# Kernel optimization log

Measured on AMD Instinct MI355X. Metric: run time of the kernel, lower is better.

Reference implementation:

```python
import jax, jax.numpy as jnp
import numpy as np

N_NODES = 50000
EPS_NORM = 1e-12
EPS_ENT = 1e-8

def _l2norm(x):
    # torch.nn.functional.normalize: x / clamp(||x||, min=1e-12)
    n = jnp.sqrt(jnp.sum(x * x, axis=-1, keepdims=True))
    return x / jnp.maximum(n, EPS_NORM)

def _layer(hidden, src, dst, edge_type, multi_emb, proto_emb):
    # hidden: [N,H]; multi_emb: [R,P,H]; proto_emb: [P,H]
    inp_j = hidden[src]                          # [E,H] gather
    rel_basis = multi_emb[edge_type]             # [E,P,H] gather
    sims = jnp.einsum('eh,ph->ep', _l2norm(inp_j), _l2norm(proto_emb))  # cosine sim [E,P]
    proto_proba = jax.nn.softmax(sims, axis=1)   # [E,P]
    msg = jnp.einsum('ep,eph->eh', proto_proba, rel_basis)              # [E,H]
    ent = -jnp.sum(proto_proba * jnp.log(proto_proba + EPS_ENT), axis=1)  # [E]
    logits = -ent
    # scatter_softmax over destination index
    seg_max = jax.ops.segment_max(logits, dst, num_segments=N_NODES)
    ex = jnp.exp(logits - seg_max[dst])
    denom = jax.ops.segment_sum(ex, dst, num_segments=N_NODES)
    attn = ex / denom[dst]                       # [E]
    out = jax.ops.segment_sum(attn[:, None] * msg, dst, num_segments=N_NODES)  # [N,H]
    return out

def setup_inputs() -> dict:
    key = jax.random.key(0)
    ks = jax.random.split(key, 6)
    E = 800000
    H, R, P, L = 128, 18, 18, 3  # num_layers=4 -> 3 NBFCluttr layers
    edge_index = jax.random.randint(ks[0], (2, E), 0, N_NODES, dtype=jnp.int64) if jax.config.read('jax_enable_x64') else jax.random.randint(ks[0], (2, E), 0, N_NODES, dtype=jnp.int32)
    edge_type = jax.random.randint(ks[1], (E,), 0, R, dtype=edge_index.dtype)
    tail_indices = jax.random.randint(ks[2], (1024,), 0, N_NODES, dtype=edge_index.dtype)
    multi_embeddings = jax.random.uniform(ks[3], (L, R, P, H), dtype=jnp.float32)
    proto_embeddings = jax.random.uniform(ks[4], (L, P, H), dtype=jnp.float32)
    source_embedding = jax.random.uniform(ks[5], (H,), dtype=jnp.float32)
    return {"edge_index": edge_index, "edge_type": edge_type, "tail_indices": tail_indices,
            "multi_embeddings": multi_embeddings, "proto_embeddings": proto_embeddings,
            "source_embedding": source_embedding}

def reference(edge_index, edge_type, tail_indices, multi_embeddings, proto_embeddings, source_embedding):
    src, dst = edge_index[0], edge_index[1]
    H = source_embedding.shape[0]
    # boundary condition: source node gets source_embedding, rest zero
    hidden = jnp.zeros((N_NODES, H), dtype=source_embedding.dtype).at[0].set(source_embedding)
    L = multi_embeddings.shape[0]
    for l in range(L):  # small fixed loop over structurally distinct layers
        hidden = _layer(hidden, src, dst, edge_type, multi_embeddings[l], proto_embeddings[l])
    # apply_classifier, eval_mode=True, use_mlp_classifier=False -> cosine sims to last layer prototypes
    out_emb = hidden[tail_indices]               # [B,H]
    sims = jnp.einsum('nh,ph->np', _l2norm(out_emb), _l2norm(proto_embeddings[-1]))
    return sims  # gumbel_softmax_sample with eval_mode=True returns logits unchanged
```

## Files before the change

kernel.cpp:

```cpp
#include <hip/hip_runtime.h>
#include <hip/hip_bf16.h>


#define N_NODES 50000
#define H 128
#define P 18
#define RP 324
#define KPAD 352
#define K0PAD 32
#define ELLW 64
#define NPART 8
#define NODES_PER_PART 6250
#define PREP_MAIN_BLOCKS 384
#define PREP_PN_BLOCKS 14
#define PREP_GS_BLOCKS 162
#define N0CAP 1024
#define NEED_CAP 20480

typedef _Float16 half8 __attribute__((ext_vector_type(8)));
typedef _Float16 half2v __attribute__((ext_vector_type(2)));
typedef float floatx4 __attribute__((ext_vector_type(4)));

__global__ __launch_bounds__(256) void ell_kernel(const int* __restrict__ src,
                                                  const int* __restrict__ dst,
                                                  const int* __restrict__ etype,
                                                  unsigned* __restrict__ cur,
                                                  unsigned* __restrict__ ep,
                                                  unsigned* __restrict__ n0list, int E) {
  int part = blockIdx.x & (NPART - 1);
  int i = (blockIdx.x >> 3) * 256 + threadIdx.x;
  if (i >= E) return;
  int d = dst[i];
  int lo = part * NODES_PER_PART;
  if (d < lo || d >= lo + NODES_PER_PART) return;
  int s = src[i];
  int r = etype[i];
  unsigned pos = atomicAdd(&cur[d], 1u);
  if (pos < ELLW)
    ep[(size_t)d * ELLW + pos] = (unsigned)s | ((unsigned)r << 20);
  if (s == 0) {
    unsigned ix = atomicAdd(&cur[N_NODES], 1u);
    if (ix < N0CAP) n0list[ix] = (unsigned)d | ((unsigned)r << 20);
  }
}

__global__ __launch_bounds__(256) void need_kernel(const int* __restrict__ tl,
                                                   const unsigned* __restrict__ ep,
                                                   unsigned* __restrict__ cur,
                                                   unsigned* __restrict__ nflag,
                                                   unsigned* __restrict__ needlist, int T) {
  int wave = threadIdx.x >> 6, lane = threadIdx.x & 63;
  int t = blockIdx.x * 4 + wave;
  if (t >= T) return;
  int nd = tl[t];
  int cnt = (int)cur[nd];
  if (cnt > ELLW) cnt = ELLW;
  if (lane < cnt) {
    unsigned s = ep[(size_t)nd * ELLW + lane] & 0xFFFFFu;
    if (atomicExch(&nflag[s], 1u) == 0u) {
      unsigned ix = atomicAdd(&cur[N_NODES + 1], 1u);
      if (ix < NEED_CAP) needlist[ix] = s;
    }
  }
}

__global__ __launch_bounds__(256) void prep_kernel(const float* __restrict__ multi,
                                                   const float* __restrict__ proto,
                                                   const float* __restrict__ semb,
                                                   float* __restrict__ pN,
                                                   _Float16* __restrict__ Btg,
                                                   _Float16* __restrict__ Btl0,
                                                   _Float16* __restrict__ BtD,
                                                   float* __restrict__ GS,
                                                   unsigned* __restrict__ cur,
                                                   unsigned* __restrict__ nflag) {
  int bid = blockIdx.x;
  if (bid >= PREP_MAIN_BLOCKS + PREP_PN_BLOCKS) {
    int wave = threadIdx.x >> 6, lane = threadIdx.x & 63;
    int pi = (bid - PREP_MAIN_BLOCKS - PREP_PN_BLOCKS) * 4 + wave;
    if (pi >= 648) return;
    float pr = 1.f / 18.f, ent0 = 0.f;
#pragma unroll
    for (int p = 0; p < P; p++) ent0 -= pr * __logf(pr + 1e-8f);
    float qc = __expf(-ent0) * pr;
    bool isG = pi < 324;
    int rr = isG ? pi / P : (pi - 324) / P;
    int cc = isG ? pi - rr * P : (pi - 324) - rr * P;
    float ca = 0.f, cb = 0.f;
#pragma unroll
    for (int q2 = 0; q2 < P; q2++) {
      ca += multi[(rr * P + q2) * H + lane];
      cb += multi[(rr * P + q2) * H + lane + 64];
    }
    ca *= qc; cb *= qc;
    float xa, xb, rn = 0.f;
    if (isG) {
      xa = proto[(P + cc) * H + lane];
      xb = proto[(P + cc) * H + lane + 64];
      rn = xa * xa + xb * xb;
    } else {
      xa = 0.f; xb = 0.f;
#pragma unroll
      for (int q2 = 0; q2 < P; q2++) {
        xa += multi[(cc * P + q2) * H + lane];
        xb += multi[(cc * P + q2) * H + lane + 64];
      }
      xa *= qc; xb *= qc;
    }
    float dotp = ca * xa + cb * xb;
    for (int m = 32; m > 0; m >>= 1) {
      dotp += __shfl_xor(dotp, m, 64);
      rn += __shfl_xor(rn, m, 64);
    }
    float val = isG ? dotp / fmaxf(sqrtf(rn), 1e-12f) : dotp;
    if (lane == 0) GS[pi] = val;
    return;
  }
  if (bid >= PREP_MAIN_BLOCKS) {
    int wave = threadIdx.x >> 6, l = threadIdx.x & 63;
    int row = (bid - PREP_MAIN_BLOCKS) * 4 + wave;
    if (row >= 54) return;
    float a = proto[row * H + l], b = proto[row * H + 64 + l];
    float ss = a * a + b * b;
    for (int m = 32; m > 0; m >>= 1) ss += __shfl_xor(ss, m, 64);
    float inv = 1.f / fmaxf(sqrtf(ss), 1e-12f);
    pN[row * H + l] = a * inv;
    pN[row * H + 64 + l] = b * inv;
    return;
  }
  int idx = bid * 256 + threadIdx.x;
  if (idx <= N_NODES + 1) cur[idx] = 0u;
  if (idx < N_NODES) nflag[idx] = 0u;
  if (idx < 2 * H * KPAD) {
    int l = idx / (H * KPAD), rem = idx - l * (H * KPAD);
    int h = rem / KPAD, k = rem - h * KPAD;
    const float* B = multi + (size_t)(l + 1) * RP * H;
    Btg[idx] = (k < RP) ? (_Float16)B[k * H + h] : (_Float16)0.f;
    return;
  }
  int idx2 = idx - 2 * H * KPAD;
  if (idx2 >= H * 64) return;
  int h = idx2 >> 6, k = idx2 & 63;
  float s0 = semb[k], s1 = semb[k + 64];
  float ssq = s0 * s0 + s1 * s1;
  float dq[P];
#pragma unroll
  for (int p = 0; p < P; p++) {
    float a = proto[p * H + k], b = proto[p * H + 64 + k];
    float rn = a * a + b * b;
    for (int m = 32; m > 0; m >>= 1) rn += __shfl_xor(rn, m, 64);
    float rinv = 1.f / fmaxf(sqrtf(rn), 1e-12f);
    dq[p] = (s0 * a + s1 * b) * rinv;
  }
  for (int m = 1; m <= 32; m <<= 1) {
    ssq += __shfl_xor(ssq, m, 64);
#pragma unroll
    for (int p = 0; p < P; p++) dq[p] += __shfl_xor(dq[p], m, 64);
  }
  float inv = 1.f / fmaxf(sqrtf(ssq), 1e-12f);
  float sum = 0.f;
#pragma unroll
  for (int p = 0; p < P; p++) {
    dq[p] = __expf(dq[p] * inv - 1.f);
    sum += dq[p];
  }
  float isum = 1.f / sum, ent = 0.f;
#pragma unroll
  for (int p = 0; p < P; p++) {
    dq[p] *= isum;
    ent -= dq[p] * __logf(dq[p] + 1e-8f);
  }
  float w = __expf(-ent);
  float pr = 1.f / 18.f, ent0 = 0.f;
#pragma unroll
  for (int p = 0; p < P; p++) ent0 -= pr * __logf(pr + 1e-8f);
  float qc = __expf(-ent0) * pr;
  if (k < K0PAD) {
    float v = 0.f;
    if (k < P) {
#pragma unroll
      for (int p = 0; p < P; p++) v += qc * multi[(k * P + p) * H + h];
    }
    Btl0[h * K0PAD + k] = (_Float16)v;
  } else if (k < K0PAD + P) {
    int r = k - K0PAD;
    float v = 0.f;
#pragma unroll
    for (int p = 0; p < P; p++) v += (w * dq[p] - qc) * multi[(r * P + p) * H + h];
    BtD[r * H + h] = (_Float16)v;
  }
}

__global__ __launch_bounds__(256) void histq_kernel(const unsigned* __restrict__ ep,
                                                    const unsigned* __restrict__ cur,
                                                    const float* __restrict__ GS,
                                                    _Float16* __restrict__ q, int n) {
  __shared__ float gs[648];
  for (int i = threadIdx.x; i < 648; i += 256) gs[i] = GS[i];
  __syncthreads();
  int wave = threadIdx.x >> 6, lane = threadIdx.x & 63;
  int nd = blockIdx.x * 4 + wave;
  if (nd >= n) return;
  int cnt = (int)cur[nd];
  if (cnt > ELLW) cnt = ELLW;
  bool a = lane < cnt;
  unsigned pk = a ? ep[(size_t)nd * ELLW + lane] : 0xFFFFFFFFu;
  int r = (int)(pk >> 20);
  float creg = 0.f;
#pragma unroll
  for (int rr = 0; rr < P; rr++) {
    unsigned long long m = __ballot(a && (r == rr));
    if (lane == rr) creg = (float)__popcll(m);
  }
  float dot = 0.f, t = 0.f;
#pragma unroll
  for (int rr = 0; rr < P; rr++) {
    float c = __shfl(creg, rr, 64);
    if (lane < P) {
      dot += c * gs[rr * P + lane];
      t += c * gs[324 + rr * P + lane];
    }
  }
  float u = (lane < P) ? creg * t : 0.f;
  for (int m = 1; m <= 16; m <<= 1) u += __shfl_xor(u, m, 32);
  float ss = u;
  float inv = 1.f / fmaxf(sqrtf(ss), 1e-12f);
  float e = (lane < P) ? __expf(dot * inv - 1.f) : 0.f;
  float sum = e;
  for (int m = 1; m <= 16; m <<= 1) sum += __shfl_xor(sum, m, 32);
  float prb = e / sum;
  float term = (lane < P) ? prb * __logf(prb + 1e-8f) : 0.f;
  float ent = term;
  for (int m = 1; m <= 16; m <<= 1) ent += __shfl_xor(ent, m, 32);
  float w = __expf(ent);
  if (lane < P) q[(size_t)nd * P + lane] = (_Float16)(w * prb);
}

__global__ __launch_bounds__(256) void patch_kernel(const unsigned* __restrict__ cur,
                                                    const unsigned* __restrict__ n0list,
                                                    const unsigned* __restrict__ ep,
                                                    const _Float16* __restrict__ Btl0,
                                                    const _Float16* __restrict__ BtD,
                                                    const float* __restrict__ pN,
                                                    _Float16* __restrict__ q) {
  int n0 = (int)cur[N_NODES];
  if (n0 > N0CAP) n0 = N0CAP;
  int wave = threadIdx.x >> 6, lane = threadIdx.x & 63;
  int e = blockIdx.x * 4 + wave;
  if (e >= n0) return;
  unsigned pe = n0list[e];
  int d = (int)(pe & 0xFFFFFu);
  for (int e2 = 0; e2 < e; e2++)
    if ((int)(n0list[e2] & 0xFFFFFu) == d) return;
  int cnt = (int)cur[d];
  if (cnt > ELLW) cnt = ELLW;
  bool a = lane < cnt;
  unsigned pk2 = a ? ep[(size_t)d * ELLW + lane] : 0xFFFFFFFFu;
  int rr0 = (int)(pk2 >> 20);
  float creg = 0.f;
#pragma unroll
  for (int rr = 0; rr < P; rr++) {
    unsigned long long m = __ballot(a && (rr0 == rr));
    if (lane == rr) creg = (float)__popcll(m);
  }
  float ya = 0.f, yb = 0.f;
#pragma unroll
  for (int rr = 0; rr < P; rr++) {
    float c = __shfl(creg, rr, 64);
    ya += c * (float)Btl0[lane * K0PAD + rr];
    yb += c * (float)Btl0[(lane + 64) * K0PAD + rr];
  }
  for (int e2 = e; e2 < n0; e2++) {
    unsigned p2 = n0list[e2];
    if ((int)(p2 & 0xFFFFFu) != d) continue;
    int r2 = (int)(p2 >> 20);
    ya += (float)BtD[r2 * H + lane];
    yb += (float)BtD[r2 * H + lane + 64];
  }
  float ss = ya * ya + yb * yb;
  float dot[P];
#pragma unroll
  for (int p = 0; p < P; p++) dot[p] = ya * pN[p * H + lane] + yb * pN[p * H + lane + 64];
  for (int m = 1; m <= 32; m <<= 1) {
    ss += __shfl_xor(ss, m, 64);
#pragma unroll
    for (int p = 0; p < P; p++) dot[p] += __shfl_xor(dot[p], m, 64);
  }
  float inv = 1.f / fmaxf(sqrtf(ss), 1e-12f);
  float sum = 0.f;
#pragma unroll
  for (int p = 0; p < P; p++) {
    dot[p] = __expf(dot[p] * inv - 1.f);
    sum += dot[p];
  }
  float isum = 1.f / sum, ent = 0.f;
#pragma unroll
  for (int p = 0; p < P; p++) {
    dot[p] *= isum;
    ent -= dot[p] * __logf(dot[p] + 1e-8f);
  }
  float w = __expf(-ent);
  if (lane < P) q[(size_t)d * P + lane] = (_Float16)(w * dot[lane]);
}

__global__ __launch_bounds__(256) void scatter_kernel(const unsigned* __restrict__ ep,
                                                      const unsigned* __restrict__ cur,
                                                      const _Float16* __restrict__ q,
                                                      const int* __restrict__ tl,
                                                      const unsigned* __restrict__ dc,
                                                      _Float16* __restrict__ M, int n) {
  __shared__ float sl[4][3 * RP];
  int wave = threadIdx.x >> 6, lane = threadIdx.x & 63;
  int t = blockIdx.x * 4 + wave;
  int neff = n;
  if (dc) {
    int c = (int)dc[0];
    if (c < neff) neff = c;
  }
  float* s0 = sl[wave];
  for (int i = lane; i < 3 * RP; i += 64) s0[i] = 0.f;
  int sub = lane / 18;
  int j = lane - sub * 18;
  bool act = (sub < 3) && (t < neff);
  int cnt = 0;
  size_t b = 0;
  if (t < neff) {
    int nd = tl ? tl[t] : t;
    b = (size_t)nd * ELLW;
    cnt = (int)cur[nd];
    if (cnt > ELLW) cnt = ELLW;
  }
  float* ms = s0 + (sub < 3 ? sub : 0) * RP;
  for (int it = 0; it < cnt; it += 18) {
    bool aa[6];
    unsigned pk[6];
    float qv[6];
#pragma unroll
    for (int u = 0; u < 6; u++) {
      int e = it + 3 * u + sub;
      aa[u] = act && (e < cnt);
      pk[u] = aa[u] ? ep[b + e] : 0u;
    }
#pragma unroll
    for (int u = 0; u < 6; u++)
      qv[u] = aa[u] ? (float)q[(size_t)(pk[u] & 0xFFFFFu) * P + j] : 0.f;
#pragma unroll
    for (int u = 0; u < 6; u++)
      if (aa[u]) ms[(pk[u] >> 20) * P + j] += qv[u];
  }
  if (t < neff) {
    for (int wd = lane; wd < RP / 2; wd += 64) {
      float2 x0 = *(const float2*)(s0 + 2 * wd);
      float2 x1 = *(const float2*)(s0 + RP + 2 * wd);
      float2 x2 = *(const float2*)(s0 + 2 * RP + 2 * wd);
      half2v hv;
      hv[0] = (_Float16)(x0.x + x1.x + x2.x);
      hv[1] = (_Float16)(x0.y + x1.y + x2.y);
      *(half2v*)(M + (size_t)t * KPAD + 2 * wd) = hv;
    }
    for (int wd = RP / 2 + lane; wd < KPAD / 2; wd += 64) {
      half2v z = {};
      *(half2v*)(M + (size_t)t * KPAD + 2 * wd) = z;
    }
  }
}

template <int MODE>
__global__ __launch_bounds__(256) void gemm_kernel(const _Float16* __restrict__ M,
                                                   const _Float16* __restrict__ Bt,
                                                   const float* __restrict__ pN,
                                                   const int* __restrict__ map,
                                                   const unsigned* __restrict__ dc,
                                                   void* __restrict__ out_ptr, int n,
                                                   int kpad) {
  int neff = n;
  if (dc) {
    int c = (int)dc[0];
    if (c < neff) neff = c;
  }
  int n0 = blockIdx.x * 64;
  if (n0 >= neff) return;
  __shared__ float smem_f[64 * 132];
  _Float16* As = (_Float16*)smem_f;
  _Float16* Bs = (_Float16*)(smem_f + 1024);
  int tid = threadIdx.x;
  int wave = tid >> 6, lane = tid & 63;
  int m15 = lane & 15, quad = lane >> 4;
  floatx4 acc[4][2] = {};

  __shared__ float pns[4 * P * 36];
  for (int i = tid; i < 4 * P * 32; i += 256) {
    int s = i / (P * 32), r = i - s * (P * 32);
    int p = r >> 5, kk = r & 31;
    pns[s * (P * 36) + p * 36 + kk] = pN[p * H + s * 32 + kk];
  }

  for (int kt = 0; kt < (kpad >> 5); kt++) {
    int k0 = kt * 32;
    __syncthreads();
    {
      int row = tid >> 2, kc = (tid & 3) * 8;
      int gr = n0 + row;
      half8 v = {};
      if (gr < neff) v = *(const half8*)(M + (size_t)gr * kpad + k0 + kc);
      *(half8*)(As + row * 32 + kc) = v;
    }
    {
      int col = tid >> 1, kc = (tid & 1) * 16;
      const _Float16* srcp = Bt + (size_t)col * kpad + k0 + kc;
      *(half8*)(Bs + col * 32 + kc) = *(const half8*)srcp;
      *(half8*)(Bs + col * 32 + kc + 8) = *(const half8*)(srcp + 8);
    }
    __syncthreads();
    half8 bfrag0 = *(const half8*)(Bs + (wave * 32 + m15) * 32 + quad * 8);
    half8 bfrag1 = *(const half8*)(Bs + (wave * 32 + 16 + m15) * 32 + quad * 8);
#pragma unroll
    for (int mt = 0; mt < 4; mt++) {
      half8 afrag = *(const half8*)(As + (mt * 16 + m15) * 32 + quad * 8);
      acc[mt][0] = __builtin_amdgcn_mfma_f32_16x16x32_f16(afrag, bfrag0, acc[mt][0], 0, 0, 0);
      acc[mt][1] = __builtin_amdgcn_mfma_f32_16x16x32_f16(afrag, bfrag1, acc[mt][1], 0, 0, 0);
    }
  }
  __syncthreads();
#pragma unroll
  for (int mt = 0; mt < 4; mt++)
#pragma unroll
    for (int c = 0; c < 2; c++)
#pragma unroll
      for (int reg = 0; reg < 4; reg++)
        smem_f[(mt * 16 + quad * 4 + reg) * 132 + wave * 32 + c * 16 + m15] = acc[mt][c][reg];
  __syncthreads();
  int node = tid >> 2, sub = tid & 3;
  int gnode = n0 + node;
  const float* trow = smem_f + node * 132 + sub * 32;
  const float* ps = pns + sub * (P * 36);
  float ss = 0.f;
  float dot[P];
#pragma unroll
  for (int p = 0; p < P; p++) dot[p] = 0.f;
#pragma unroll
  for (int k4 = 0; k4 < 8; k4++) {
    float4 y = *(const float4*)(trow + k4 * 4);
    ss += y.x * y.x + y.y * y.y + y.z * y.z + y.w * y.w;
#pragma unroll
    for (int p = 0; p < P; p++) {
      float4 b = *(const float4*)(ps + p * 36 + k4 * 4);
      dot[p] += y.x * b.x + y.y * b.y + y.z * b.z + y.w * b.w;
    }
  }
  for (int m = 1; m <= 2; m <<= 1) {
    ss += __shfl_xor(ss, m, 64);
#pragma unroll
    for (int p = 0; p < P; p++) dot[p] += __shfl_xor(dot[p], m, 64);
  }
  if (gnode < neff) {
    float inv = 1.f / fmaxf(sqrtf(ss), 1e-12f);
    if (MODE == 1) {
      float* outp = (float*)out_ptr;
      for (int p = sub; p < P; p += 4) outp[(size_t)gnode * P + p] = dot[p] * inv;
    } else {
      float sum = 0.f;
#pragma unroll
      for (int p = 0; p < P; p++) {
        dot[p] = __expf(dot[p] * inv - 1.f);
        sum += dot[p];
      }
      float isum = 1.f / sum, ent = 0.f;
#pragma unroll
      for (int p = 0; p < P; p++) {
        dot[p] *= isum;
        ent -= dot[p] * __logf(dot[p] + 1e-8f);
      }
      float w = __expf(-ent);
      int gout = map ? map[gnode] : gnode;
      _Float16* qp = (_Float16*)out_ptr;
      for (int p = sub; p < P; p += 4) qp[(size_t)gout * P + p] = (_Float16)(w * dot[p]);
    }
  }
}

extern "C" void kernel_launch(void* const* d_in, const int* in_sizes, int n_in,
                              void* d_out, int out_size, void* d_ws, size_t ws_size,
                              hipStream_t stream) {
  const int* eidx = (const int*)d_in[0];
  int E = in_sizes[0] / 2;
  const int* src = eidx;
  const int* dst = eidx + E;
  const int* etype = (const int*)d_in[1];
  const int* tails = (const int*)d_in[2];
  int T = in_sizes[2];
  const float* multi = (const float*)d_in[3];
  const float* proto = (const float*)d_in[4];
  const float* semb = (const float*)d_in[5];
  float* out = (float*)d_out;

  char* w = (char*)d_ws;
  auto alloc = [&](size_t bytes) {
    char* p = w;
    w += (bytes + 255) & ~(size_t)255;
    return p;
  };
  _Float16* q = (_Float16*)alloc((size_t)N_NODES * P * 2);
  float* pNs = (float*)alloc((size_t)3 * P * H * 4);
  float* GS = (float*)alloc((size_t)648 * 4);
  _Float16* Mg = (_Float16*)alloc((size_t)N_NODES * KPAD * 2);
  _Float16* Btg = (_Float16*)alloc((size_t)2 * H * KPAD * 2);
  _Float16* Btl0 = (_Float16*)alloc((size_t)H * K0PAD * 2);
  _Float16* BtD = (_Float16*)alloc((size_t)P * H * 2);
  unsigned* cur = (unsigned*)alloc((size_t)(N_NODES + 2) * 4);
  unsigned* n0list = (unsigned*)alloc((size_t)N0CAP * 4);
  unsigned* nflag = (unsigned*)alloc((size_t)N_NODES * 4);
  unsigned* needlist = (unsigned*)alloc((size_t)NEED_CAP * 4);
  unsigned* ep = (unsigned*)alloc((size_t)N_NODES * ELLW * 4);

  int eb = (E + 255) / 256;
  const unsigned* needcnt = cur + N_NODES + 1;

  prep_kernel<<<PREP_MAIN_BLOCKS + PREP_PN_BLOCKS + PREP_GS_BLOCKS, 256, 0, stream>>>(
      multi, proto, semb, pNs, Btg, Btl0, BtD, GS, cur, nflag);

  ell_kernel<<<eb * NPART, 256, 0, stream>>>(src, dst, etype, cur, ep, n0list, E);

  histq_kernel<<<(N_NODES + 3) / 4, 256, 0, stream>>>(ep, cur, GS, q, N_NODES);
  patch_kernel<<<(N0CAP + 3) / 4, 256, 0, stream>>>(cur, n0list, ep, Btl0, BtD,
                                                    pNs + (size_t)1 * P * H, q);

  need_kernel<<<(T + 3) / 4, 256, 0, stream>>>(tails, ep, cur, nflag, needlist, T);

  scatter_kernel<<<(NEED_CAP + 3) / 4, 256, 0, stream>>>(ep, cur, q, (const int*)needlist,
                                                         needcnt, Mg, NEED_CAP);
  gemm_kernel<0><<<(NEED_CAP + 63) / 64, 256, 0, stream>>>(
      Mg, Btg, pNs + (size_t)2 * P * H, (const int*)needlist, needcnt, q, NEED_CAP, KPAD);

  scatter_kernel<<<(T + 3) / 4, 256, 0, stream>>>(ep, cur, q, tails, nullptr, Mg, T);
  gemm_kernel<1><<<(T + 63) / 64, 256, 0, stream>>>(Mg, Btg + (size_t)H * KPAD,
                                                    pNs + (size_t)2 * P * H, nullptr, nullptr,
                                                    out, T, KPAD);
}
```

Baseline: 214.3 us.

## Replace full ELL build with per-node relation histogram and targeted ELL passes

Drops the 8-way partitioned full ELL construction. A per-node edge-type histogram is now built with atomics and feeds histq and patch directly. Full ELL adjacency is built only for tail nodes in a first edge pass and for their needed source nodes in a second pass. This cuts the scattered ELL writes and the 8x re-reading of the edge arrays, at the cost of two full edge passes, histogram atomics and a larger zeroing step in prep.

```diff
diff --git a/kernel.cpp b/kernel.cpp
--- a/kernel.cpp
+++ b/kernel.cpp
@@ -9,11 +9,10 @@
 #define KPAD 352
 #define K0PAD 32
 #define ELLW 64
-#define NPART 8
-#define NODES_PER_PART 6250
-#define PREP_MAIN_BLOCKS 384
+#define PREP_MAIN_BLOCKS 880
 #define PREP_PN_BLOCKS 14
 #define PREP_GS_BLOCKS 162
+#define HIST4_WORDS 225000
 #define N0CAP 1024
 #define NEED_CAP 20480
 
@@ -21,23 +20,30 @@
 typedef _Float16 half2v __attribute__((ext_vector_type(2)));
 typedef float floatx4 __attribute__((ext_vector_type(4)));
 
-__global__ __launch_bounds__(256) void ell_kernel(const int* __restrict__ src,
-                                                  const int* __restrict__ dst,
-                                                  const int* __restrict__ etype,
-                                                  unsigned* __restrict__ cur,
-                                                  unsigned* __restrict__ ep,
-                                                  unsigned* __restrict__ n0list, int E) {
-  int part = blockIdx.x & (NPART - 1);
-  int i = (blockIdx.x >> 3) * 256 + threadIdx.x;
+__global__ __launch_bounds__(256) void tflag_kernel(const int* __restrict__ tl,
+                                                    unsigned* __restrict__ tflag, int T) {
+  int i = blockIdx.x * 256 + threadIdx.x;
+  if (i < T) tflag[tl[i]] = 1u;
+}
+
+__global__ __launch_bounds__(256) void edge1_kernel(const int* __restrict__ src,
+                                                    const int* __restrict__ dst,
+                                                    const int* __restrict__ etype,
+                                                    const unsigned* __restrict__ tflag,
+                                                    unsigned* __restrict__ cur,
+                                                    unsigned* __restrict__ hist,
+                                                    unsigned* __restrict__ ep,
+                                                    unsigned* __restrict__ n0list, int E) {
+  int i = blockIdx.x * 256 + threadIdx.x;
   if (i >= E) return;
   int d = dst[i];
-  int lo = part * NODES_PER_PART;
-  if (d < lo || d >= lo + NODES_PER_PART) return;
   int s = src[i];
   int r = etype[i];
-  unsigned pos = atomicAdd(&cur[d], 1u);
-  if (pos < ELLW)
-    ep[(size_t)d * ELLW + pos] = (unsigned)s | ((unsigned)r << 20);
+  atomicAdd(&hist[(size_t)d * P + r], 1u);
+  if (tflag[d]) {
+    unsigned pos = atomicAdd(&cur[d], 1u);
+    if (pos < ELLW) ep[(size_t)d * ELLW + pos] = (unsigned)s | ((unsigned)r << 20);
+  }
   if (s == 0) {
     unsigned ix = atomicAdd(&cur[N_NODES], 1u);
     if (ix < N0CAP) n0list[ix] = (unsigned)d | ((unsigned)r << 20);
@@ -64,6 +70,23 @@
   }
 }
 
+__global__ __launch_bounds__(256) void edge2_kernel(const int* __restrict__ src,
+                                                    const int* __restrict__ dst,
+                                                    const int* __restrict__ etype,
+                                                    const unsigned* __restrict__ nflag,
+                                                    const unsigned* __restrict__ tflag,
+                                                    unsigned* __restrict__ cur,
+                                                    unsigned* __restrict__ ep, int E) {
+  int i = blockIdx.x * 256 + threadIdx.x;
+  if (i >= E) return;
+  int d = dst[i];
+  if (!nflag[d] || tflag[d]) return;
+  int s = src[i];
+  int r = etype[i];
+  unsigned pos = atomicAdd(&cur[d], 1u);
+  if (pos < ELLW) ep[(size_t)d * ELLW + pos] = (unsigned)s | ((unsigned)r << 20);
+}
+
 __global__ __launch_bounds__(256) void prep_kernel(const float* __restrict__ multi,
                                                    const float* __restrict__ proto,
                                                    const float* __restrict__ semb,
@@ -73,7 +96,9 @@
                                                    _Float16* __restrict__ BtD,
                                                    float* __restrict__ GS,
                                                    unsigned* __restrict__ cur,
-                                                   unsigned* __restrict__ nflag) {
+                                                   unsigned* __restrict__ nflag,
+                                                   unsigned* __restrict__ tflag,
+                                                   uint4* __restrict__ hist4) {
   int bid = blockIdx.x;
   if (bid >= PREP_MAIN_BLOCKS + PREP_PN_BLOCKS) {
     int wave = threadIdx.x >> 6, lane = threadIdx.x & 63;
@@ -130,7 +155,14 @@
   }
   int idx = bid * 256 + threadIdx.x;
   if (idx <= N_NODES + 1) cur[idx] = 0u;
-  if (idx < N_NODES) nflag[idx] = 0u;
+  if (idx < N_NODES) {
+    nflag[idx] = 0u;
+    tflag[idx] = 0u;
+  }
+  if (idx < HIST4_WORDS) {
+    uint4 z = {0u, 0u, 0u, 0u};
+    hist4[idx] = z;
+  }
   if (idx < 2 * H * KPAD) {
     int l = idx / (H * KPAD), rem = idx - l * (H * KPAD);
     int h = rem / KPAD, k = rem - h * KPAD;
@@ -191,8 +223,7 @@
   }
 }
 
-__global__ __launch_bounds__(256) void histq_kernel(const unsigned* __restrict__ ep,
-                                                    const unsigned* __restrict__ cur,
+__global__ __launch_bounds__(256) void histq_kernel(const unsigned* __restrict__ hist,
                                                     const float* __restrict__ GS,
                                                     _Float16* __restrict__ q, int n) {
   __shared__ float gs[648];
@@ -201,17 +232,7 @@
   int wave = threadIdx.x >> 6, lane = threadIdx.x & 63;
   int nd = blockIdx.x * 4 + wave;
   if (nd >= n) return;
-  int cnt = (int)cur[nd];
-  if (cnt > ELLW) cnt = ELLW;
-  bool a = lane < cnt;
-  unsigned pk = a ? ep[(size_t)nd * ELLW + lane] : 0xFFFFFFFFu;
-  int r = (int)(pk >> 20);
-  float creg = 0.f;
-#pragma unroll
-  for (int rr = 0; rr < P; rr++) {
-    unsigned long long m = __ballot(a && (r == rr));
-    if (lane == rr) creg = (float)__popcll(m);
-  }
+  float creg = (lane < P) ? (float)hist[(size_t)nd * P + lane] : 0.f;
   float dot = 0.f, t = 0.f;
 #pragma unroll
   for (int rr = 0; rr < P; rr++) {
@@ -238,7 +259,7 @@
 
 __global__ __launch_bounds__(256) void patch_kernel(const unsigned* __restrict__ cur,
                                                     const unsigned* __restrict__ n0list,
-                                                    const unsigned* __restrict__ ep,
+                                                    const unsigned* __restrict__ hist,
                                                     const _Float16* __restrict__ Btl0,
                                                     const _Float16* __restrict__ BtD,
                                                     const float* __restrict__ pN,
@@ -252,17 +273,7 @@
   int d = (int)(pe & 0xFFFFFu);
   for (int e2 = 0; e2 < e; e2++)
     if ((int)(n0list[e2] & 0xFFFFFu) == d) return;
-  int cnt = (int)cur[d];
-  if (cnt > ELLW) cnt = ELLW;
-  bool a = lane < cnt;
-  unsigned pk2 = a ? ep[(size_t)d * ELLW + lane] : 0xFFFFFFFFu;
-  int rr0 = (int)(pk2 >> 20);
-  float creg = 0.f;
-#pragma unroll
-  for (int rr = 0; rr < P; rr++) {
-    unsigned long long m = __ballot(a && (rr0 == rr));
-    if (lane == rr) creg = (float)__popcll(m);
-  }
+  float creg = (lane < P) ? (float)hist[(size_t)d * P + lane] : 0.f;
   float ya = 0.f, yb = 0.f;
 #pragma unroll
   for (int rr = 0; rr < P; rr++) {
@@ -510,22 +521,27 @@
   unsigned* cur = (unsigned*)alloc((size_t)(N_NODES + 2) * 4);
   unsigned* n0list = (unsigned*)alloc((size_t)N0CAP * 4);
   unsigned* nflag = (unsigned*)alloc((size_t)N_NODES * 4);
+  unsigned* tflag = (unsigned*)alloc((size_t)N_NODES * 4);
   unsigned* needlist = (unsigned*)alloc((size_t)NEED_CAP * 4);
+  unsigned* hist = (unsigned*)alloc((size_t)N_NODES * P * 4);
   unsigned* ep = (unsigned*)alloc((size_t)N_NODES * ELLW * 4);
 
   int eb = (E + 255) / 256;
   const unsigned* needcnt = cur + N_NODES + 1;
 
   prep_kernel<<<PREP_MAIN_BLOCKS + PREP_PN_BLOCKS + PREP_GS_BLOCKS, 256, 0, stream>>>(
-      multi, proto, semb, pNs, Btg, Btl0, BtD, GS, cur, nflag);
-
-  ell_kernel<<<eb * NPART, 256, 0, stream>>>(src, dst, etype, cur, ep, n0list, E);
-
-  histq_kernel<<<(N_NODES + 3) / 4, 256, 0, stream>>>(ep, cur, GS, q, N_NODES);
-  patch_kernel<<<(N0CAP + 3) / 4, 256, 0, stream>>>(cur, n0list, ep, Btl0, BtD,
+      multi, proto, semb, pNs, Btg, Btl0, BtD, GS, cur, nflag, tflag, (uint4*)hist);
+  tflag_kernel<<<(T + 255) / 256, 256, 0, stream>>>(tails, tflag, T);
+
+  edge1_kernel<<<eb, 256, 0, stream>>>(src, dst, etype, tflag, cur, hist, ep, n0list, E);
+
+  need_kernel<<<(T + 3) / 4, 256, 0, stream>>>(tails, ep, cur, nflag, needlist, T);
+
+  edge2_kernel<<<eb, 256, 0, stream>>>(src, dst, etype, nflag, tflag, cur, ep, E);
+
+  histq_kernel<<<(N_NODES + 3) / 4, 256, 0, stream>>>(hist, GS, q, N_NODES);
+  patch_kernel<<<(N0CAP + 3) / 4, 256, 0, stream>>>(cur, n0list, hist, Btl0, BtD,
                                                     pNs + (size_t)1 * P * H, q);
-
-  need_kernel<<<(T + 3) / 4, 256, 0, stream>>>(tails, ep, cur, nflag, needlist, T);
 
   scatter_kernel<<<(NEED_CAP + 3) / 4, 256, 0, stream>>>(ep, cur, q, (const int*)needlist,
                                                          needcnt, Mg, NEED_CAP);
```

Measured after the change: 226.1 us. 1.06x slower.
